# Performance work log

Measured on AMD Instinct MI355X. Metric: run time of the kernel, lower is better.

Reference implementation:

```python
import jax, jax.numpy as jnp
import numpy as np

N = 80000; E = 1280000; IN = 128; H1 = 128; H2 = 128; H3 = 64
L1D = 512; L2D = 256; OUT = 10; K = 2; GROUP = 40


def setup_inputs() -> dict:
    key = jax.random.key(0)
    ks = jax.random.split(key, 16)
    s = 0.05
    d = {}
    d['x'] = jax.random.normal(ks[0], (N, IN), jnp.float32)
    d['edge_index'] = jax.random.randint(ks[1], (2, E), 0, N, jnp.int32)
    # SGConv linears (applied after K-hop propagation)
    d['W1'] = jax.random.normal(ks[2], (H1, IN), jnp.float32) * s
    d['b1'] = jnp.zeros((H1,), jnp.float32)
    d['W2'] = jax.random.normal(ks[3], (H2, H1), jnp.float32) * s
    d['b2'] = jnp.zeros((H2,), jnp.float32)
    # GATConv (heads=1)
    d['Wg'] = jax.random.normal(ks[4], (H3, H2), jnp.float32) * s
    d['att_src'] = jax.random.normal(ks[5], (H3,), jnp.float32) * s
    d['att_dst'] = jax.random.normal(ks[6], (H3,), jnp.float32) * s
    d['bg'] = jnp.zeros((H3,), jnp.float32)
    # MLP head
    d['L1'] = jax.random.normal(ks[7], (L1D, H3 * GROUP), jnp.float32) * s
    d['bl1'] = jnp.zeros((L1D,), jnp.float32)
    d['L2'] = jax.random.normal(ks[8], (L2D, L1D), jnp.float32) * s
    d['bl2'] = jnp.zeros((L2D,), jnp.float32)
    d['L3'] = jax.random.normal(ks[9], (OUT, L2D), jnp.float32) * s
    d['bl3'] = jnp.zeros((OUT,), jnp.float32)
    return d


def _lrelu(v, slope=0.1):
    return jnp.where(v > 0, v, slope * v)


def _forward(x, src, dst, norm, W1, b1, W2, b2, Wg, bg, att_src, att_dst,
             L1, bl1, L2, bl2, L3, bl3):
    # SGConv: x <- S^K x, then linear. S = D^-1/2 (A+I) D^-1/2
    def prop(h):
        return jax.ops.segment_sum(norm[:, None] * h[src], dst, num_segments=N)

    h = x
    for _ in range(K):
        h = prop(h)
    h = _lrelu(h @ W1.T + b1)
    for _ in range(K):
        h = prop(h)
    h = _lrelu(h @ W2.T + b2)

    # GATConv (1 head), self-loops included in (src, dst)
    g = h @ Wg.T                                   # [N, H3]
    a_s = g @ att_src                              # [N]
    a_d = g @ att_dst                              # [N]
    e = _lrelu(a_s[src] + a_d[dst], 0.2)           # [E+N]
    emax = jax.ops.segment_max(e, dst, num_segments=N)
    ee = jnp.exp(e - emax[dst])
    den = jax.ops.segment_sum(ee, dst, num_segments=N)
    alpha = ee / den[dst]
    h = jax.ops.segment_sum(alpha[:, None] * g[src], dst, num_segments=N) + bg
    h = _lrelu(h)

    # pool 40-node groups, MLP head
    h = h.reshape(N // GROUP, H3 * GROUP)
    h = _lrelu(h @ L1.T + bl1)
    h = _lrelu(h @ L2.T + bl2)
    h = _lrelu(h @ L3.T + bl3)
    return h


def reference(x, edge_index, W1, b1, W2, b2, Wg, bg, att_src, att_dst,
              L1, bl1, L2, bl2, L3, bl3):
    loops = jnp.arange(N, dtype=edge_index.dtype)
    src = jnp.concatenate([edge_index[0], loops])
    dst = jnp.concatenate([edge_index[1], loops])
    deg = jax.ops.segment_sum(jnp.ones_like(src, jnp.float32), dst, num_segments=N)
    dinv = jnp.where(deg > 0, jax.lax.rsqrt(deg), 0.0)
    norm = dinv[src] * dinv[dst]
    return _forward(x, src, dst, norm, W1, b1, W2, b2, Wg, bg, att_src,
                    att_dst, L1, bl1, L2, bl2, L3, bl3)
```

## Files before the change

kernel.cpp:

```cpp
#include <hip/hip_runtime.h>

#define N_NODES 80000
#define N_EDGES 1280000
#define NNZ (N_EDGES + N_NODES)
#define DIM 128
#define HD3 64
#define GROUP 40
#define NPOOL (N_NODES / GROUP)
#define L1DIM 512
#define L2DIM 256
#define OUTD 10
#define SPLITK 4
#define L1K (HD3 * GROUP)

#define SCAN_BLK 1024
#define SCAN_NB ((N_NODES + SCAN_BLK - 1) / SCAN_BLK)

#define NB_BUCKETS ((N_NODES + 255) >> 8)
#define NB_PAD 320
#define EPB 8192
#define NBLK ((NNZ + EPB - 1) / EPB)

#define QX  (N_NODES * DIM / 4)
#define QW1 (DIM * DIM / 4)
#define QW2 (DIM * DIM / 4)
#define QWG (HD3 * DIM / 4)
#define QL1 (L1DIM * L1K / 4)
#define QTOT (QX + QW1 + QW2 + QWG + QL1)

typedef unsigned int u32;
typedef unsigned short u16;
typedef __bf16 bf16x8 __attribute__((ext_vector_type(8)));
typedef float f32x4 __attribute__((ext_vector_type(4)));
typedef float f32x2 __attribute__((ext_vector_type(2)));

__device__ __forceinline__ float lrelu(float v, float s) { return v > 0.f ? v : s * v; }

__device__ __forceinline__ float b2f(u16 b) {
    u32 u = ((u32)b) << 16;
    float f; __builtin_memcpy(&f, &u, 4); return f;
}
__device__ __forceinline__ u16 f2b(float f) {
    u32 u; __builtin_memcpy(&u, &f, 4);
    return (u16)((u + 0x7fffu + ((u >> 16) & 1u)) >> 16);
}
__device__ __forceinline__ f32x2 bf2(u32 v) {
    f32x2 r;
    r.x = __uint_as_float(v << 16);
    r.y = __uint_as_float(v & 0xffff0000u);
    return r;
}


__global__ __launch_bounds__(256) void k_hist(const int* __restrict__ ei, u32* __restrict__ cnt) {
    __shared__ u32 h[NB_PAD];
    for (int i = threadIdx.x; i < NB_PAD; i += 256) h[i] = 0;
    __syncthreads();
    int base = blockIdx.x * EPB;
    #pragma unroll 4
    for (int i = 0; i < EPB / 256; ++i) {
        int idx = base + i * 256 + threadIdx.x;
        if (idx < NNZ) {
            int d = (idx < N_EDGES) ? ei[N_EDGES + idx] : idx - N_EDGES;
            atomicAdd(&h[d >> 8], 1u);
        }
    }
    __syncthreads();
    for (int b = threadIdx.x; b < NB_BUCKETS; b += 256)
        cnt[blockIdx.x * NB_PAD + b] = h[b];
}

__global__ __launch_bounds__(256) void k_bscan_col(const u32* __restrict__ cnt,
                                                   u32* __restrict__ basep,
                                                   u32* __restrict__ btot) {
    int b = blockIdx.x, t = threadIdx.x;
    u32 v = (t < NBLK) ? cnt[t * NB_PAD + b] : 0;
    __shared__ u32 sm[256];
    sm[t] = v; __syncthreads();
    for (int off = 1; off < 256; off <<= 1) {
        u32 u = (t >= off) ? sm[t - off] : 0; __syncthreads();
        sm[t] += u; __syncthreads();
    }
    if (t < NBLK) basep[t * NB_PAD + b] = sm[t] - v;
    if (t == 255) btot[b] = sm[255];
}

__global__ __launch_bounds__(512) void k_bscan_top(const u32* __restrict__ btot,
                                                   u32* __restrict__ bbase) {
    __shared__ u32 sm[512];
    int t = threadIdx.x;
    u32 v = (t < NB_BUCKETS) ? btot[t] : 0;
    sm[t] = v; __syncthreads();
    for (int off = 1; off < 512; off <<= 1) {
        u32 u = (t >= off) ? sm[t - off] : 0; __syncthreads();
        sm[t] += u; __syncthreads();
    }
    if (t < NB_BUCKETS) bbase[t] = sm[t] - v;
    if (t == NB_BUCKETS - 1) bbase[NB_BUCKETS] = sm[t];
}

__global__ __launch_bounds__(256) void k_binscatter(const int* __restrict__ ei,
                                                    const u32* __restrict__ basep,
                                                    const u32* __restrict__ bbase,
                                                    u32* __restrict__ pairs) {
    __shared__ u32 rk[NB_PAD];
    for (int i = threadIdx.x; i < NB_PAD; i += 256) rk[i] = 0;
    __syncthreads();
    int base = blockIdx.x * EPB;
    #pragma unroll 4
    for (int i = 0; i < EPB / 256; ++i) {
        int idx = base + i * 256 + threadIdx.x;
        if (idx < NNZ) {
            int s, d;
            if (idx < N_EDGES) { s = ei[idx]; d = ei[N_EDGES + idx]; }
            else { s = idx - N_EDGES; d = s; }
            int b = d >> 8;
            u32 r = atomicAdd(&rk[b], 1u);
            u32 pos = bbase[b] + basep[blockIdx.x * NB_PAD + b] + r;
            pairs[pos] = ((u32)(d & 255) << 24) | (u32)s;
        }
    }
}

__global__ __launch_bounds__(256) void k_count2(const u32* __restrict__ pairs,
                                                const u32* __restrict__ bbase,
                                                int* __restrict__ indeg) {
    __shared__ u32 c[256];
    c[threadIdx.x] = 0;
    __syncthreads();
    int b = blockIdx.x;
    int lo = bbase[b], hi = bbase[b + 1];
    for (int i = lo + threadIdx.x; i < hi; i += 256)
        atomicAdd(&c[pairs[i] >> 24], 1u);
    __syncthreads();
    int node = (b << 8) + threadIdx.x;
    if (node < N_NODES) indeg[node] = (int)c[threadIdx.x];
}

__global__ __launch_bounds__(256) void k_fill2(const u32* __restrict__ pairs,
                                               const u32* __restrict__ bbase,
                                               const int* __restrict__ row_ptr,
                                               int* __restrict__ col_src) {
    __shared__ u32 c[256];
    c[threadIdx.x] = 0;
    __syncthreads();
    int b = blockIdx.x;
    int lo = bbase[b], hi = bbase[b + 1];
    for (int i = lo + threadIdx.x; i < hi; i += 256) {
        u32 p = pairs[i];
        u32 dl = p >> 24;
        int dst = (b << 8) + (int)dl;
        u32 r = atomicAdd(&c[dl], 1u);
        col_src[row_ptr[dst] + r] = (int)(p & 0xFFFFFFu);
    }
}


__global__ __launch_bounds__(256) void k_scan_reduce(const int* __restrict__ indeg,
                                                     int* __restrict__ part) {
    int base = blockIdx.x * SCAN_BLK + threadIdx.x * 4;
    int s = 0;
    if (base < N_NODES) {
        int4 v = *(const int4*)(indeg + base);
        s = v.x + v.y + v.z + v.w;
    }
    for (int off = 32; off; off >>= 1) s += __shfl_xor(s, off);
    __shared__ int sm[4];
    if ((threadIdx.x & 63) == 0) sm[threadIdx.x >> 6] = s;
    __syncthreads();
    if (threadIdx.x == 0) part[blockIdx.x] = sm[0] + sm[1] + sm[2] + sm[3];
}

__global__ __launch_bounds__(128) void k_scan_top(const int* __restrict__ part,
                                                  int* __restrict__ poff,
                                                  int* __restrict__ row_ptr) {
    __shared__ int sm[128];
    int t = threadIdx.x;
    int v = (t < SCAN_NB) ? part[t] : 0;
    sm[t] = v;
    __syncthreads();
    for (int off = 1; off < 128; off <<= 1) {
        int u = (t >= off) ? sm[t - off] : 0;
        __syncthreads();
        sm[t] += u;
        __syncthreads();
    }
    if (t < SCAN_NB) poff[t] = sm[t] - v;
    if (t == 0) row_ptr[N_NODES] = NNZ;
}

__global__ __launch_bounds__(256) void k_scan_apply(const int* __restrict__ indeg,
                                                    const int* __restrict__ poff,
                                                    int* __restrict__ row_ptr,
                                                    float* __restrict__ dinv) {
    int t = threadIdx.x;
    int base = blockIdx.x * SCAN_BLK + t * 4;
    int4 v = {0, 0, 0, 0};
    if (base < N_NODES) v = *(const int4*)(indeg + base);
    int tot = v.x + v.y + v.z + v.w;
    __shared__ int sm[256];
    sm[t] = tot;
    __syncthreads();
    for (int off = 1; off < 256; off <<= 1) {
        int u = (t >= off) ? sm[t - off] : 0;
        __syncthreads();
        sm[t] += u;
        __syncthreads();
    }
    if (base >= N_NODES) return;
    int excl = sm[t] - tot + poff[blockIdx.x];
    int4 p = make_int4(excl, excl + v.x, excl + v.x + v.y, excl + v.x + v.y + v.z);
    *(int4*)(row_ptr + base) = p;
    float4 dv = make_float4(rsqrtf((float)v.x), rsqrtf((float)v.y),
                            rsqrtf((float)v.z), rsqrtf((float)v.w));
    *(float4*)(dinv + base) = dv;
}


__global__ __launch_bounds__(256) void k_f2b_all(const float* __restrict__ x,   u16* __restrict__ xb,
                                                 const float* __restrict__ w1,  u16* __restrict__ w1b,
                                                 const float* __restrict__ w2,  u16* __restrict__ w2b,
                                                 const float* __restrict__ wg,  u16* __restrict__ wgb,
                                                 const float* __restrict__ l1,  u16* __restrict__ l1b) {
    int i = blockIdx.x * blockDim.x + threadIdx.x;
    const float* src; u16* dst; int off;
    if (i < QX)                      { src = x;  dst = xb;  off = i; }
    else if (i < QX + QW1)           { src = w1; dst = w1b; off = i - QX; }
    else if (i < QX + QW1 + QW2)     { src = w2; dst = w2b; off = i - QX - QW1; }
    else if (i < QX + QW1 + QW2 + QWG) { src = wg; dst = wgb; off = i - QX - QW1 - QW2; }
    else if (i < QTOT)               { src = l1; dst = l1b; off = i - QX - QW1 - QW2 - QWG; }
    else return;
    float4 v = ((const float4*)src)[off];
    ushort4 o = { f2b(v.x), f2b(v.y), f2b(v.z), f2b(v.w) };
    ((ushort4*)dst)[off] = o;
}


__global__ __launch_bounds__(256) void k_prop_bf(const int* __restrict__ row_ptr,
                                                 const int* __restrict__ col_src,
                                                 const float* __restrict__ dinv,
                                                 const u16* __restrict__ hin,
                                                 u16* __restrict__ hout) {
    int lane = threadIdx.x & 63;
    int node = blockIdx.x * 4 + (threadIdx.x >> 6);
    if (node >= N_NODES) return;
    int j0 = row_ptr[node], j1 = row_ptr[node + 1];
    float dn = dinv[node];
    const int grp = lane >> 4;
    const int dl  = lane & 15;
    f32x2 acc[4] = {};

    for (int base = j0; base < j1; base += 64) {
        int cnt = j1 - base; if (cnt > 64) cnt = 64;
        int jj = base + lane;
        int sidx = (jj < j1) ? col_src[jj] : 0;
        int l = 0;
        for (; l + 16 <= cnt; l += 16) {
            uint4 v[4]; f32x2 w2[4];
            #pragma unroll
            for (int q = 0; q < 4; ++q) {
                int s = __shfl(sidx, l + q * 4 + grp);
                float wq = dinv[s] * dn;
                w2[q].x = wq; w2[q].y = wq;
                v[q] = *(const uint4*)(hin + (size_t)s * DIM + dl * 8);
            }
            #pragma unroll
            for (int q = 0; q < 4; ++q) {
                acc[0] = __builtin_elementwise_fma(bf2(v[q].x), w2[q], acc[0]);
                acc[1] = __builtin_elementwise_fma(bf2(v[q].y), w2[q], acc[1]);
                acc[2] = __builtin_elementwise_fma(bf2(v[q].z), w2[q], acc[2]);
                acc[3] = __builtin_elementwise_fma(bf2(v[q].w), w2[q], acc[3]);
            }
        }
        for (; l + 4 <= cnt; l += 4) {
            int s = __shfl(sidx, l + grp);
            float wq = dinv[s] * dn;
            f32x2 w2; w2.x = wq; w2.y = wq;
            uint4 v = *(const uint4*)(hin + (size_t)s * DIM + dl * 8);
            acc[0] = __builtin_elementwise_fma(bf2(v.x), w2, acc[0]);
            acc[1] = __builtin_elementwise_fma(bf2(v.y), w2, acc[1]);
            acc[2] = __builtin_elementwise_fma(bf2(v.z), w2, acc[2]);
            acc[3] = __builtin_elementwise_fma(bf2(v.w), w2, acc[3]);
        }
        for (; l < cnt; ++l) {
            int s = __shfl(sidx, l);
            if (grp == 0) {
                float wq = dinv[s] * dn;
                f32x2 w2; w2.x = wq; w2.y = wq;
                uint4 v = *(const uint4*)(hin + (size_t)s * DIM + dl * 8);
                acc[0] = __builtin_elementwise_fma(bf2(v.x), w2, acc[0]);
                acc[1] = __builtin_elementwise_fma(bf2(v.y), w2, acc[1]);
                acc[2] = __builtin_elementwise_fma(bf2(v.z), w2, acc[2]);
                acc[3] = __builtin_elementwise_fma(bf2(v.w), w2, acc[3]);
            }
        }
    }
    #pragma unroll
    for (int d = 0; d < 4; ++d) {
        acc[d].x += __shfl_xor(acc[d].x, 16); acc[d].x += __shfl_xor(acc[d].x, 32);
        acc[d].y += __shfl_xor(acc[d].y, 16); acc[d].y += __shfl_xor(acc[d].y, 32);
    }
    if (grp == 0) {
        uint4 o;
        o.x = (u32)f2b(acc[0].x) | ((u32)f2b(acc[0].y) << 16);
        o.y = (u32)f2b(acc[1].x) | ((u32)f2b(acc[1].y) << 16);
        o.z = (u32)f2b(acc[2].x) | ((u32)f2b(acc[2].y) << 16);
        o.w = (u32)f2b(acc[3].x) | ((u32)f2b(acc[3].y) << 16);
        *(uint4*)(hout + (size_t)node * DIM + dl * 8) = o;
    }
}


template<int NT, bool BIAS, bool ACT>
__global__ __launch_bounds__(256) void k_gemm_mfma(const u16* __restrict__ A,
                                                   const u16* __restrict__ Wb,
                                                   const float* __restrict__ b,
                                                   u16* __restrict__ C,
                                                   int M, int K) {
    const int lane = threadIdx.x & 63;
    const int wave = threadIdx.x >> 6;
    const int m0 = blockIdx.x * 64 + wave * 16;
    const int row = lane & 15, kg = lane >> 4;
    const int Ntot = NT * 16;

    const u16* Ap = A + (size_t)(m0 + row) * K + kg * 8;
    f32x4 acc[NT] = {};

    for (int k0 = 0; k0 < K; k0 += 32) {
        bf16x8 a = *(const bf16x8*)(Ap + k0);
        #pragma unroll
        for (int nt = 0; nt < NT; ++nt) {
            const u16* Wp = Wb + (size_t)(nt * 16 + row) * K + k0 + kg * 8;
            bf16x8 bb = *(const bf16x8*)Wp;
            acc[nt] = __builtin_amdgcn_mfma_f32_16x16x32_bf16(a, bb, acc[nt], 0, 0, 0);
        }
    }

    #pragma unroll
    for (int nt = 0; nt < NT; ++nt) {
        float bias = BIAS ? b[nt * 16 + row] : 0.f;
        #pragma unroll
        for (int r = 0; r < 4; ++r) {
            float v = acc[nt][r] + bias;
            if (ACT) v = lrelu(v, 0.1f);
            int crow = m0 + kg * 4 + r;
            C[(size_t)crow * Ntot + nt * 16 + row] = f2b(v);
        }
    }
}


template<int NT>
__global__ __launch_bounds__(256) void k_gemm_mfma_sk(const u16* __restrict__ A,
                                                      const u16* __restrict__ Wb,
                                                      float* __restrict__ C,
                                                      int M, int Ntot, int K, int kChunk) {
    const int lane = threadIdx.x & 63;
    const int wave = threadIdx.x >> 6;
    const int m0 = blockIdx.x * 64 + wave * 16;
    const int row = lane & 15, kg = lane >> 4;
    const int n0 = blockIdx.y * NT * 16;
    const int kBeg = blockIdx.z * kChunk;

    int arow = m0 + row; if (arow >= M) arow = M - 1;
    const u16* Ap = A + (size_t)arow * K + kg * 8;
    f32x4 acc[NT] = {};

    for (int k0 = kBeg; k0 < kBeg + kChunk; k0 += 32) {
        bf16x8 a = *(const bf16x8*)(Ap + k0);
        #pragma unroll
        for (int nt = 0; nt < NT; ++nt) {
            const u16* Wp = Wb + (size_t)(n0 + nt * 16 + row) * K + k0 + kg * 8;
            bf16x8 bb = *(const bf16x8*)Wp;
            acc[nt] = __builtin_amdgcn_mfma_f32_16x16x32_bf16(a, bb, acc[nt], 0, 0, 0);
        }
    }

    float* Cp = C + (size_t)blockIdx.z * M * Ntot;
    #pragma unroll
    for (int nt = 0; nt < NT; ++nt) {
        #pragma unroll
        for (int r = 0; r < 4; ++r) {
            int crow = m0 + kg * 4 + r;
            if (crow < M) Cp[(size_t)crow * Ntot + n0 + nt * 16 + row] = acc[nt][r];
        }
    }
}


template<int BM, int BN, int BK, int TM, int TN, bool BIAS, bool ACT>
__global__ __launch_bounds__(256) void k_gemm(const float* __restrict__ A,
                                              const float* __restrict__ W,
                                              const float* __restrict__ b,
                                              float* __restrict__ C,
                                              int M, int Ntot, int K) {
    __shared__ float As[BK][BM + 4];
    __shared__ float Bs[BK][BN + 4];
    const int t = threadIdx.x;
    const int m0 = blockIdx.x * BM, n0 = blockIdx.y * BN;
    const int ty = t / (BN / TN), tx = t % (BN / TN);

    float acc[TM][TN] = {};

    for (int k0 = 0; k0 < K; k0 += BK) {
        #pragma unroll
        for (int p = 0; p < BM * BK / 4 / 256; ++p) {
            int id = p * 256 + t;
            int m = id % BM, kk = (id / BM) * 4;
            float4 v = {0.f, 0.f, 0.f, 0.f};
            if (m0 + m < M) v = *(const float4*)(A + (size_t)(m0 + m) * K + k0 + kk);
            As[kk + 0][m] = v.x; As[kk + 1][m] = v.y;
            As[kk + 2][m] = v.z; As[kk + 3][m] = v.w;
        }
        #pragma unroll
        for (int p = 0; p < BN * BK / 4 / 256; ++p) {
            int id = p * 256 + t;
            int n = id % BN, kk = (id / BN) * 4;
            float4 v = *(const float4*)(W + (size_t)(n0 + n) * K + k0 + kk);
            Bs[kk + 0][n] = v.x; Bs[kk + 1][n] = v.y;
            Bs[kk + 2][n] = v.z; Bs[kk + 3][n] = v.w;
        }
        __syncthreads();

        #pragma unroll
        for (int k = 0; k < BK; ++k) {
            float a[TM], bb[TN];
            #pragma unroll
            for (int i = 0; i < TM; ++i) a[i] = As[k][ty * TM + i];
            #pragma unroll
            for (int j = 0; j < TN; ++j) bb[j] = Bs[k][tx * TN + j];
            #pragma unroll
            for (int i = 0; i < TM; ++i)
                #pragma unroll
                for (int j = 0; j < TN; ++j)
                    acc[i][j] += a[i] * bb[j];
        }
        __syncthreads();
    }

    #pragma unroll
    for (int i = 0; i < TM; ++i) {
        int row = m0 + ty * TM + i;
        if (row >= M) continue;
        float4 o;
        float* op = (float*)&o;
        #pragma unroll
        for (int j = 0; j < TN; ++j) {
            float r = acc[i][j];
            if (BIAS) r += b[n0 + tx * TN + j];
            if (ACT) r = lrelu(r, 0.1f);
            op[j] = r;
        }
        *(float4*)(C + (size_t)row * Ntot + n0 + tx * TN) = o;
    }
}

__global__ __launch_bounds__(256) void k_splitk_reduce(const float* __restrict__ part,
                                                       const float* __restrict__ b,
                                                       float* __restrict__ out) {
    const int total4 = NPOOL * L1DIM / 4;
    int idx = blockIdx.x * blockDim.x + threadIdx.x;
    if (idx >= total4) return;
    const size_t stride4 = (size_t)NPOOL * L1DIM / 4;
    const float4* p4 = (const float4*)part;
    float4 s = p4[idx];
    #pragma unroll
    for (int z = 1; z < SPLITK; ++z) {
        float4 v = p4[idx + z * stride4];
        s.x += v.x; s.y += v.y; s.z += v.z; s.w += v.w;
    }
    int col = (idx * 4) % L1DIM;
    float4 bb = *(const float4*)(b + col);
    s.x = lrelu(s.x + bb.x, 0.1f); s.y = lrelu(s.y + bb.y, 0.1f);
    s.z = lrelu(s.z + bb.z, 0.1f); s.w = lrelu(s.w + bb.w, 0.1f);
    ((float4*)out)[idx] = s;
}


template<int KD, int OD, bool BIAS, bool ACT>
__global__ void k_linear(const float* __restrict__ in, const float* __restrict__ W,
                         const float* __restrict__ b, float* __restrict__ out, int nrows) {
    int idx = blockIdx.x * blockDim.x + threadIdx.x;
    int n = idx / OD, o = idx % OD;
    if (n >= nrows) return;
    const float4* ar = (const float4*)(in + (size_t)n * KD);
    const float4* wr = (const float4*)(W + (size_t)o * KD);
    float4 acc = {0.f, 0.f, 0.f, 0.f};
    #pragma unroll 8
    for (int k = 0; k < KD / 4; ++k) {
        float4 a = ar[k], w = wr[k];
        acc.x += a.x * w.x; acc.y += a.y * w.y;
        acc.z += a.z * w.z; acc.w += a.w * w.w;
    }
    float r = (acc.x + acc.y) + (acc.z + acc.w);
    if (BIAS) r += b[o];
    if (ACT) r = lrelu(r, 0.1f);
    out[idx] = r;
}


__global__ __launch_bounds__(256) void k_attn(const u16* __restrict__ g,
                                              const float* __restrict__ att_src,
                                              const float* __restrict__ att_dst,
                                              float* __restrict__ a_s, float* __restrict__ a_d) {
    int lane = threadIdx.x & 63;
    int node = blockIdx.x * 4 + (threadIdx.x >> 6);
    if (node >= N_NODES) return;
    float v = b2f(g[(size_t)node * HD3 + lane]);
    float s1 = v * att_src[lane];
    float s2 = v * att_dst[lane];
    for (int off = 32; off; off >>= 1) {
        s1 += __shfl_xor(s1, off);
        s2 += __shfl_xor(s2, off);
    }
    if (lane == 0) { a_s[node] = s1; a_d[node] = s2; }
}


__global__ __launch_bounds__(256) void k_gat(const int* __restrict__ row_ptr,
                                             const int* __restrict__ col_src,
                                             const u16* __restrict__ g,
                                             const float* __restrict__ a_s,
                                             const float* __restrict__ a_d,
                                             const float* __restrict__ bg,
                                             u16* __restrict__ hout) {
    __shared__ float wbuf[4][64];
    int lane = threadIdx.x & 63;
    int wid  = threadIdx.x >> 6;
    int node = blockIdx.x * 4 + wid;
    if (node >= N_NODES) return;
    int j0 = row_ptr[node], j1 = row_ptr[node + 1];
    float ad = a_d[node];
    const int grp = lane >> 4, dl = lane & 15;
    float m = -1e30f, den = 0.f;
    f32x2 acc[2] = {};

    for (int base = j0; base < j1; base += 64) {
        int cnt = j1 - base; if (cnt > 64) cnt = 64;
        int jj = base + lane;
        int sidx = 0;
        float e = -1e30f;
        if (jj < j1) { sidx = col_src[jj]; e = lrelu(a_s[sidx] + ad, 0.2f); }
        float cm = e;
        for (int off = 32; off; off >>= 1) cm = fmaxf(cm, __shfl_xor(cm, off));
        float nm = fmaxf(m, cm);
        float scale = __expf(m - nm);
        float wv = (jj < j1) ? __expf(e - nm) : 0.f;
        wbuf[wid][lane] = wv;
        float cden = wv;
        for (int off = 32; off; off >>= 1) cden += __shfl_xor(cden, off);
        den = den * scale + cden;
        f32x2 sc2; sc2.x = scale; sc2.y = scale;
        acc[0] *= sc2; acc[1] *= sc2;
        m = nm;
        int l = 0;
        for (; l + 16 <= cnt; l += 16) {
            uint2 v[4]; f32x2 w2[4];
            #pragma unroll
            for (int q = 0; q < 4; ++q) {
                int e2 = l + q * 4 + grp;
                int s = __shfl(sidx, e2);
                float wq = wbuf[wid][e2];
                w2[q].x = wq; w2[q].y = wq;
                v[q] = *(const uint2*)(g + (size_t)s * HD3 + dl * 4);
            }
            #pragma unroll
            for (int q = 0; q < 4; ++q) {
                acc[0] = __builtin_elementwise_fma(bf2(v[q].x), w2[q], acc[0]);
                acc[1] = __builtin_elementwise_fma(bf2(v[q].y), w2[q], acc[1]);
            }
        }
        for (; l + 4 <= cnt; l += 4) {
            int e2 = l + grp;
            int s = __shfl(sidx, e2);
            float wq = wbuf[wid][e2];
            f32x2 w2; w2.x = wq; w2.y = wq;
            uint2 v = *(const uint2*)(g + (size_t)s * HD3 + dl * 4);
            acc[0] = __builtin_elementwise_fma(bf2(v.x), w2, acc[0]);
            acc[1] = __builtin_elementwise_fma(bf2(v.y), w2, acc[1]);
        }
        for (; l < cnt; ++l) {
            int s = __shfl(sidx, l);
            if (grp == 0) {
                float wq = wbuf[wid][l];
                f32x2 w2; w2.x = wq; w2.y = wq;
                uint2 v = *(const uint2*)(g + (size_t)s * HD3 + dl * 4);
                acc[0] = __builtin_elementwise_fma(bf2(v.x), w2, acc[0]);
                acc[1] = __builtin_elementwise_fma(bf2(v.y), w2, acc[1]);
            }
        }
    }
    #pragma unroll
    for (int d = 0; d < 2; ++d) {
        acc[d].x += __shfl_xor(acc[d].x, 16); acc[d].x += __shfl_xor(acc[d].x, 32);
        acc[d].y += __shfl_xor(acc[d].y, 16); acc[d].y += __shfl_xor(acc[d].y, 32);
    }
    if (grp == 0) {
        float r0 = lrelu(acc[0].x / den + bg[dl * 4 + 0], 0.1f);
        float r1 = lrelu(acc[0].y / den + bg[dl * 4 + 1], 0.1f);
        float r2 = lrelu(acc[1].x / den + bg[dl * 4 + 2], 0.1f);
        float r3 = lrelu(acc[1].y / den + bg[dl * 4 + 3], 0.1f);
        uint2 o;
        o.x = (u32)f2b(r0) | ((u32)f2b(r1) << 16);
        o.y = (u32)f2b(r2) | ((u32)f2b(r3) << 16);
        *(uint2*)(hout + (size_t)node * HD3 + dl * 4) = o;
    }
}


extern "C" void kernel_launch(void* const* d_in, const int* in_sizes, int n_in,
                              void* d_out, int out_size, void* d_ws, size_t ws_size,
                              hipStream_t stream) {
    const float* x   = (const float*)d_in[0];
    const int*   ei  = (const int*)d_in[1];
    const float* W1  = (const float*)d_in[2];
    const float* b1  = (const float*)d_in[3];
    const float* W2  = (const float*)d_in[4];
    const float* b2  = (const float*)d_in[5];
    const float* Wg  = (const float*)d_in[6];
    const float* att_src = (const float*)d_in[7];
    const float* att_dst = (const float*)d_in[8];
    const float* bg  = (const float*)d_in[9];
    const float* L1  = (const float*)d_in[10];
    const float* bl1 = (const float*)d_in[11];
    const float* L2  = (const float*)d_in[12];
    const float* bl2 = (const float*)d_in[13];
    const float* L3  = (const float*)d_in[14];
    const float* bl3 = (const float*)d_in[15];
    float* out = (float*)d_out;

    char* w = (char*)d_ws;
    auto alloc = [&](size_t bytes) {
        char* p = w;
        w += (bytes + 255) & ~(size_t)255;
        return p;
    };
    int*   indeg    = (int*)alloc((size_t)N_NODES * 4);
    int*   row_ptr  = (int*)alloc((size_t)(N_NODES + 1) * 4);
    float* dinv     = (float*)alloc((size_t)N_NODES * 4);
    int*   col_src  = (int*)alloc((size_t)NNZ * 4);
    u32*   pairs    = (u32*)alloc((size_t)NNZ * 4);
    u32*   cnt      = (u32*)alloc((size_t)NBLK * NB_PAD * 4);
    u32*   basep    = (u32*)alloc((size_t)NBLK * NB_PAD * 4);
    u32*   btot     = (u32*)alloc((size_t)NB_PAD * 4);
    u32*   bbase    = (u32*)alloc((size_t)(NB_BUCKETS + 1) * 4);
    u16*   bufX     = (u16*)alloc((size_t)N_NODES * DIM * 2);
    u16*   bufA     = (u16*)alloc((size_t)N_NODES * DIM * 2);
    u16*   bufB     = (u16*)alloc((size_t)N_NODES * DIM * 2);
    float* a_s      = (float*)alloc((size_t)N_NODES * 4);
    float* a_d      = (float*)alloc((size_t)N_NODES * 4);
    float* p1       = (float*)alloc((size_t)NPOOL * L1DIM * 4);
    float* p2       = (float*)alloc((size_t)NPOOL * L2DIM * 4);
    int*   part     = (int*)alloc((size_t)SCAN_NB * 4);
    int*   poff     = (int*)alloc((size_t)SCAN_NB * 4);
    u16*   W1b      = (u16*)alloc((size_t)DIM * DIM * 2);
    u16*   W2b      = (u16*)alloc((size_t)DIM * DIM * 2);
    u16*   Wgb      = (u16*)alloc((size_t)HD3 * DIM * 2);
    u16*   L1b      = (u16*)alloc((size_t)L1DIM * L1K * 2);
    u16*   gb    = bufX;
    u16*   hGb   = bufA;
    float* skbuf = (float*)bufB;

    dim3 b256(256);
    k_hist<<<NBLK, b256, 0, stream>>>(ei, cnt);
    k_bscan_col<<<NB_BUCKETS, b256, 0, stream>>>(cnt, basep, btot);
    k_bscan_top<<<1, 512, 0, stream>>>(btot, bbase);
    k_binscatter<<<NBLK, b256, 0, stream>>>(ei, basep, bbase, pairs);
    k_count2<<<NB_BUCKETS, b256, 0, stream>>>(pairs, bbase, indeg);
    k_scan_reduce<<<SCAN_NB, b256, 0, stream>>>(indeg, part);
    k_scan_top<<<1, 128, 0, stream>>>(part, poff, row_ptr);
    k_scan_apply<<<SCAN_NB, b256, 0, stream>>>(indeg, poff, row_ptr, dinv);
    k_fill2<<<NB_BUCKETS, b256, 0, stream>>>(pairs, bbase, row_ptr, col_src);

    k_f2b_all<<<(QTOT + 255) / 256, b256, 0, stream>>>(x, bufX, W1, W1b, W2, W2b, Wg, Wgb, L1, L1b);

    int nb = (N_NODES + 3) / 4;
    int gemm_nb = N_NODES / 64;
    k_prop_bf<<<nb, b256, 0, stream>>>(row_ptr, col_src, dinv, bufX, bufA);
    k_prop_bf<<<nb, b256, 0, stream>>>(row_ptr, col_src, dinv, bufA, bufB);
    k_gemm_mfma<8, true, true><<<gemm_nb, b256, 0, stream>>>(bufB, W1b, b1, bufA, N_NODES, DIM);
    k_prop_bf<<<nb, b256, 0, stream>>>(row_ptr, col_src, dinv, bufA, bufB);
    k_prop_bf<<<nb, b256, 0, stream>>>(row_ptr, col_src, dinv, bufB, bufA);
    k_gemm_mfma<8, true, true><<<gemm_nb, b256, 0, stream>>>(bufA, W2b, b2, bufB, N_NODES, DIM);
    k_gemm_mfma<4, false, false><<<gemm_nb, b256, 0, stream>>>(bufB, Wgb, nullptr, gb, N_NODES, DIM);
    k_attn<<<nb, b256, 0, stream>>>(gb, att_src, att_dst, a_s, a_d);
    k_gat<<<nb, b256, 0, stream>>>(row_ptr, col_src, gb, a_s, a_d, bg, hGb);
    k_gemm_mfma_sk<8><<<dim3(32, 4, SPLITK), b256, 0, stream>>>(
        hGb, L1b, skbuf, NPOOL, L1DIM, L1K, L1K / SPLITK);
    k_splitk_reduce<<<(NPOOL * L1DIM / 4 + 255) / 256, b256, 0, stream>>>(skbuf, bl1, p1);
    k_gemm<64, 64, 32, 4, 4, true, true><<<dim3(32, 4), b256, 0, stream>>>(p1, L2, bl2, p2, NPOOL, L2DIM, L1DIM);
    k_linear<256, 10, true, true><<<(NPOOL * 10 + 255) / 256, b256, 0, stream>>>(p2, L3, bl3, out, NPOOL);
}
```

Baseline: 491.5 us.

## Fuse CSR build into per-bucket kernel and fold attention dots into GEMM

Merges the degree-count, global scan and fill kernels into one per-bucket kernel. Since pairs are already bucketed by destination, each bucket's row pointers come from a local scan offset by the bucket base. It also computes the GAT attention projections a_s/a_d inside the Wg GEMM epilogue from the fp32 accumulators, removing the separate k_attn kernel and its re-read of g. This cuts several launches and memory passes. The attention scores now come from unrounded fp32 accumulators rather than bf16-rounded g, which changes numerics slightly.

```diff
diff --git a/kernel.cpp b/kernel.cpp
--- a/kernel.cpp
+++ b/kernel.cpp
@@ -13,9 +13,6 @@
 #define SPLITK 4
 #define L1K (HD3 * GROUP)
 
-#define SCAN_BLK 1024
-#define SCAN_NB ((N_NODES + SCAN_BLK - 1) / SCAN_BLK)
-
 #define NB_BUCKETS ((N_NODES + 255) >> 8)
 #define NB_PAD 320
 #define EPB 8192
@@ -86,7 +83,8 @@
 }
 
 __global__ __launch_bounds__(512) void k_bscan_top(const u32* __restrict__ btot,
-                                                   u32* __restrict__ bbase) {
+                                                   u32* __restrict__ bbase,
+                                                   int* __restrict__ row_ptr) {
     __shared__ u32 sm[512];
     int t = threadIdx.x;
     u32 v = (t < NB_BUCKETS) ? btot[t] : 0;
@@ -97,6 +95,7 @@
     }
     if (t < NB_BUCKETS) bbase[t] = sm[t] - v;
     if (t == NB_BUCKETS - 1) bbase[NB_BUCKETS] = sm[t];
+    if (t == 0) row_ptr[N_NODES] = NNZ;
 }
 
 __global__ __launch_bounds__(256) void k_binscatter(const int* __restrict__ ei,
@@ -122,98 +121,40 @@
     }
 }
 
-__global__ __launch_bounds__(256) void k_count2(const u32* __restrict__ pairs,
-                                                const u32* __restrict__ bbase,
-                                                int* __restrict__ indeg) {
-    __shared__ u32 c[256];
-    c[threadIdx.x] = 0;
+__global__ __launch_bounds__(256) void k_build_csr(const u32* __restrict__ pairs,
+                                                   const u32* __restrict__ bbase,
+                                                   int* __restrict__ row_ptr,
+                                                   float* __restrict__ dinv,
+                                                   int* __restrict__ col_src) {
+    __shared__ u32 c[256], sc[256], ex[256];
+    int t = threadIdx.x, b = blockIdx.x;
+    int lo = bbase[b], hi = bbase[b + 1];
+    c[t] = 0;
     __syncthreads();
-    int b = blockIdx.x;
-    int lo = bbase[b], hi = bbase[b + 1];
-    for (int i = lo + threadIdx.x; i < hi; i += 256)
+    for (int i = lo + t; i < hi; i += 256)
         atomicAdd(&c[pairs[i] >> 24], 1u);
     __syncthreads();
-    int node = (b << 8) + threadIdx.x;
-    if (node < N_NODES) indeg[node] = (int)c[threadIdx.x];
-}
-
-__global__ __launch_bounds__(256) void k_fill2(const u32* __restrict__ pairs,
-                                               const u32* __restrict__ bbase,
-                                               const int* __restrict__ row_ptr,
-                                               int* __restrict__ col_src) {
-    __shared__ u32 c[256];
-    c[threadIdx.x] = 0;
+    u32 cv = c[t];
+    sc[t] = cv;
     __syncthreads();
-    int b = blockIdx.x;
-    int lo = bbase[b], hi = bbase[b + 1];
-    for (int i = lo + threadIdx.x; i < hi; i += 256) {
+    for (int off = 1; off < 256; off <<= 1) {
+        u32 u = (t >= off) ? sc[t - off] : 0; __syncthreads();
+        sc[t] += u; __syncthreads();
+    }
+    ex[t] = sc[t] - cv;
+    int node = (b << 8) + t;
+    if (node < N_NODES) {
+        row_ptr[node] = lo + (int)ex[t];
+        dinv[node] = rsqrtf((float)cv);
+    }
+    c[t] = 0;
+    __syncthreads();
+    for (int i = lo + t; i < hi; i += 256) {
         u32 p = pairs[i];
         u32 dl = p >> 24;
-        int dst = (b << 8) + (int)dl;
         u32 r = atomicAdd(&c[dl], 1u);
-        col_src[row_ptr[dst] + r] = (int)(p & 0xFFFFFFu);
-    }
-}
-
-
-__global__ __launch_bounds__(256) void k_scan_reduce(const int* __restrict__ indeg,
-                                                     int* __restrict__ part) {
-    int base = blockIdx.x * SCAN_BLK + threadIdx.x * 4;
-    int s = 0;
-    if (base < N_NODES) {
-        int4 v = *(const int4*)(indeg + base);
-        s = v.x + v.y + v.z + v.w;
-    }
-    for (int off = 32; off; off >>= 1) s += __shfl_xor(s, off);
-    __shared__ int sm[4];
-    if ((threadIdx.x & 63) == 0) sm[threadIdx.x >> 6] = s;
-    __syncthreads();
-    if (threadIdx.x == 0) part[blockIdx.x] = sm[0] + sm[1] + sm[2] + sm[3];
-}
-
-__global__ __launch_bounds__(128) void k_scan_top(const int* __restrict__ part,
-                                                  int* __restrict__ poff,
-                                                  int* __restrict__ row_ptr) {
-    __shared__ int sm[128];
-    int t = threadIdx.x;
-    int v = (t < SCAN_NB) ? part[t] : 0;
-    sm[t] = v;
-    __syncthreads();
-    for (int off = 1; off < 128; off <<= 1) {
-        int u = (t >= off) ? sm[t - off] : 0;
-        __syncthreads();
-        sm[t] += u;
-        __syncthreads();
-    }
-    if (t < SCAN_NB) poff[t] = sm[t] - v;
-    if (t == 0) row_ptr[N_NODES] = NNZ;
-}
-
-__global__ __launch_bounds__(256) void k_scan_apply(const int* __restrict__ indeg,
-                                                    const int* __restrict__ poff,
-                                                    int* __restrict__ row_ptr,
-                                                    float* __restrict__ dinv) {
-    int t = threadIdx.x;
-    int base = blockIdx.x * SCAN_BLK + t * 4;
-    int4 v = {0, 0, 0, 0};
-    if (base < N_NODES) v = *(const int4*)(indeg + base);
-    int tot = v.x + v.y + v.z + v.w;
-    __shared__ int sm[256];
-    sm[t] = tot;
-    __syncthreads();
-    for (int off = 1; off < 256; off <<= 1) {
-        int u = (t >= off) ? sm[t - off] : 0;
-        __syncthreads();
-        sm[t] += u;
-        __syncthreads();
-    }
-    if (base >= N_NODES) return;
-    int excl = sm[t] - tot + poff[blockIdx.x];
-    int4 p = make_int4(excl, excl + v.x, excl + v.x + v.y, excl + v.x + v.y + v.z);
-    *(int4*)(row_ptr + base) = p;
-    float4 dv = make_float4(rsqrtf((float)v.x), rsqrtf((float)v.y),
-                            rsqrtf((float)v.z), rsqrtf((float)v.w));
-    *(float4*)(dinv + base) = dv;
+        col_src[lo + (int)ex[dl] + (int)r] = (int)(p & 0xFFFFFFu);
+    }
 }
 
 
@@ -224,11 +165,11 @@
                                                  const float* __restrict__ l1,  u16* __restrict__ l1b) {
     int i = blockIdx.x * blockDim.x + threadIdx.x;
     const float* src; u16* dst; int off;
-    if (i < QX)                      { src = x;  dst = xb;  off = i; }
-    else if (i < QX + QW1)           { src = w1; dst = w1b; off = i - QX; }
-    else if (i < QX + QW1 + QW2)     { src = w2; dst = w2b; off = i - QX - QW1; }
+    if (i < QX)                        { src = x;  dst = xb;  off = i; }
+    else if (i < QX + QW1)             { src = w1; dst = w1b; off = i - QX; }
+    else if (i < QX + QW1 + QW2)       { src = w2; dst = w2b; off = i - QX - QW1; }
     else if (i < QX + QW1 + QW2 + QWG) { src = wg; dst = wgb; off = i - QX - QW1 - QW2; }
-    else if (i < QTOT)               { src = l1; dst = l1b; off = i - QX - QW1 - QW2 - QWG; }
+    else if (i < QTOT)                 { src = l1; dst = l1b; off = i - QX - QW1 - QW2 - QWG; }
     else return;
     float4 v = ((const float4*)src)[off];
     ushort4 o = { f2b(v.x), f2b(v.y), f2b(v.z), f2b(v.w) };
@@ -311,11 +252,15 @@
 }
 
 
-template<int NT, bool BIAS, bool ACT>
+template<int NT, bool BIAS, bool ACT, bool ATTN>
 __global__ __launch_bounds__(256) void k_gemm_mfma(const u16* __restrict__ A,
                                                    const u16* __restrict__ Wb,
                                                    const float* __restrict__ b,
                                                    u16* __restrict__ C,
+                                                   const float* __restrict__ att_src,
+                                                   const float* __restrict__ att_dst,
+                                                   float* __restrict__ a_s,
+                                                   float* __restrict__ a_d,
                                                    int M, int K) {
     const int lane = threadIdx.x & 63;
     const int wave = threadIdx.x >> 6;
@@ -345,6 +290,35 @@
             if (ACT) v = lrelu(v, 0.1f);
             int crow = m0 + kg * 4 + r;
             C[(size_t)crow * Ntot + nt * 16 + row] = f2b(v);
+        }
+    }
+
+    if (ATTN) {
+        float s1[4] = {}, s2[4] = {};
+        #pragma unroll
+        for (int nt = 0; nt < NT; ++nt) {
+            float as = att_src[nt * 16 + row];
+            float av = att_dst[nt * 16 + row];
+            #pragma unroll
+            for (int r = 0; r < 4; ++r) {
+                s1[r] += acc[nt][r] * as;
+                s2[r] += acc[nt][r] * av;
+            }
+        }
+        #pragma unroll
+        for (int r = 0; r < 4; ++r) {
+            #pragma unroll
+            for (int off = 1; off < 16; off <<= 1) {
+                s1[r] += __shfl_xor(s1[r], off);
+                s2[r] += __shfl_xor(s2[r], off);
+            }
+        }
+        if (row == 0) {
+            #pragma unroll
+            for (int r = 0; r < 4; ++r) {
+                a_s[m0 + kg * 4 + r] = s1[r];
+                a_d[m0 + kg * 4 + r] = s2[r];
+            }
         }
     }
 }
@@ -496,24 +470,6 @@
     if (BIAS) r += b[o];
     if (ACT) r = lrelu(r, 0.1f);
     out[idx] = r;
-}
-
-
-__global__ __launch_bounds__(256) void k_attn(const u16* __restrict__ g,
-                                              const float* __restrict__ att_src,
-                                              const float* __restrict__ att_dst,
-                                              float* __restrict__ a_s, float* __restrict__ a_d) {
-    int lane = threadIdx.x & 63;
-    int node = blockIdx.x * 4 + (threadIdx.x >> 6);
-    if (node >= N_NODES) return;
-    float v = b2f(g[(size_t)node * HD3 + lane]);
-    float s1 = v * att_src[lane];
-    float s2 = v * att_dst[lane];
-    for (int off = 32; off; off >>= 1) {
-        s1 += __shfl_xor(s1, off);
-        s2 += __shfl_xor(s2, off);
-    }
-    if (lane == 0) { a_s[node] = s1; a_d[node] = s2; }
 }
 
 
@@ -635,7 +591,6 @@
         w += (bytes + 255) & ~(size_t)255;
         return p;
     };
-    int*   indeg    = (int*)alloc((size_t)N_NODES * 4);
     int*   row_ptr  = (int*)alloc((size_t)(N_NODES + 1) * 4);
     float* dinv     = (float*)alloc((size_t)N_NODES * 4);
     int*   col_src  = (int*)alloc((size_t)NNZ * 4);
@@ -651,8 +606,6 @@
     float* a_d      = (float*)alloc((size_t)N_NODES * 4);
     float* p1       = (float*)alloc((size_t)NPOOL * L1DIM * 4);
     float* p2       = (float*)alloc((size_t)NPOOL * L2DIM * 4);
-    int*   part     = (int*)alloc((size_t)SCAN_NB * 4);
-    int*   poff     = (int*)alloc((size_t)SCAN_NB * 4);
     u16*   W1b      = (u16*)alloc((size_t)DIM * DIM * 2);
     u16*   W2b      = (u16*)alloc((size_t)DIM * DIM * 2);
     u16*   Wgb      = (u16*)alloc((size_t)HD3 * DIM * 2);
@@ -664,13 +617,9 @@
     dim3 b256(256);
     k_hist<<<NBLK, b256, 0, stream>>>(ei, cnt);
     k_bscan_col<<<NB_BUCKETS, b256, 0, stream>>>(cnt, basep, btot);
-    k_bscan_top<<<1, 512, 0, stream>>>(btot, bbase);
+    k_bscan_top<<<1, 512, 0, stream>>>(btot, bbase, row_ptr);
     k_binscatter<<<NBLK, b256, 0, stream>>>(ei, basep, bbase, pairs);
-    k_count2<<<NB_BUCKETS, b256, 0, stream>>>(pairs, bbase, indeg);
-    k_scan_reduce<<<SCAN_NB, b256, 0, stream>>>(indeg, part);
-    k_scan_top<<<1, 128, 0, stream>>>(part, poff, row_ptr);
-    k_scan_apply<<<SCAN_NB, b256, 0, stream>>>(indeg, poff, row_ptr, dinv);
-    k_fill2<<<NB_BUCKETS, b256, 0, stream>>>(pairs, bbase, row_ptr, col_src);
+    k_build_csr<<<NB_BUCKETS, b256, 0, stream>>>(pairs, bbase, row_ptr, dinv, col_src);
 
     k_f2b_all<<<(QTOT + 255) / 256, b256, 0, stream>>>(x, bufX, W1, W1b, W2, W2b, Wg, Wgb, L1, L1b);
 
@@ -678,12 +627,14 @@
     int gemm_nb = N_NODES / 64;
     k_prop_bf<<<nb, b256, 0, stream>>>(row_ptr, col_src, dinv, bufX, bufA);
     k_prop_bf<<<nb, b256, 0, stream>>>(row_ptr, col_src, dinv, bufA, bufB);
-    k_gemm_mfma<8, true, true><<<gemm_nb, b256, 0, stream>>>(bufB, W1b, b1, bufA, N_NODES, DIM);
+    k_gemm_mfma<8, true, true, false><<<gemm_nb, b256, 0, stream>>>(
+        bufB, W1b, b1, bufA, nullptr, nullptr, nullptr, nullptr, N_NODES, DIM);
     k_prop_bf<<<nb, b256, 0, stream>>>(row_ptr, col_src, dinv, bufA, bufB);
     k_prop_bf<<<nb, b256, 0, stream>>>(row_ptr, col_src, dinv, bufB, bufA);
-    k_gemm_mfma<8, true, true><<<gemm_nb, b256, 0, stream>>>(bufA, W2b, b2, bufB, N_NODES, DIM);
-    k_gemm_mfma<4, false, false><<<gemm_nb, b256, 0, stream>>>(bufB, Wgb, nullptr, gb, N_NODES, DIM);
-    k_attn<<<nb, b256, 0, stream>>>(gb, att_src, att_dst, a_s, a_d);
+    k_gemm_mfma<8, true, true, false><<<gemm_nb, b256, 0, stream>>>(
+        bufA, W2b, b2, bufB, nullptr, nullptr, nullptr, nullptr, N_NODES, DIM);
+    k_gemm_mfma<4, false, false, true><<<gemm_nb, b256, 0, stream>>>(
+        bufB, Wgb, nullptr, gb, att_src, att_dst, a_s, a_d, N_NODES, DIM);
     k_gat<<<nb, b256, 0, stream>>>(row_ptr, col_src, gb, a_s, a_d, bg, hGb);
     k_gemm_mfma_sk<8><<<dim3(32, 4, SPLITK), b256, 0, stream>>>(
         hGb, L1b, skbuf, NPOOL, L1DIM, L1K, L1K / SPLITK);
```

Result: faster. 473.2 us, median of 2 (-3.7%).
